# Kernel tuning notes

Hardware: AMD Instinct MI355X
Metric: run time of the kernel (lower is better)

## Reference

```python
import jax, jax.numpy as jnp
import numpy as np

B = 4096
IN_DIM = 256
OUT_DIM = 256
COND_DIM = 128
HID = 512
HYPER_OUT = IN_DIM * OUT_DIM  # 65536


def setup_inputs() -> dict:
    key = jax.random.key(0)
    ks = jax.random.split(key, 8)

    def xavier(k, shape):
        fan_in, fan_out = shape[0], shape[1]
        std = np.sqrt(2.0 / (fan_in + fan_out))
        return jax.random.normal(k, shape, dtype=jnp.float32) * std

    return {
        "input_h": jax.random.normal(ks[0], (B, IN_DIM), dtype=jnp.float32),
        "condition_z": jax.random.normal(ks[1], (B, COND_DIM), dtype=jnp.float32),
        # hypernet: Linear(COND_DIM, HID) -> ReLU -> Linear(HID, HYPER_OUT)
        "W1": xavier(ks[2], (COND_DIM, HID)),
        "b1": jnp.zeros((HID,), dtype=jnp.float32),
        "W2": xavier(ks[3], (HID, HYPER_OUT)),
        "b2": jnp.zeros((HYPER_OUT,), dtype=jnp.float32),
        # static bias (use_bias=True, generate_bias=False)
        "bias": jnp.zeros((1, OUT_DIM), dtype=jnp.float32),
    }


def reference(input_h, condition_z, W1, b1, W2, b2, bias):
    # HyperNet MLP generates per-sample weight matrix
    hyp = jax.nn.relu(condition_z @ W1 + b1)          # [B, HID]
    weight_S = hyp @ W2 + b2                          # [B, IN*OUT]  (1 GB intermediate)
    weight_S = weight_S.reshape(-1, IN_DIM, OUT_DIM)  # [B, IN, OUT]
    # batched matmul: [B,1,IN] x [B,IN,OUT] -> [B,OUT]
    out = jnp.einsum("bi,bio->bo", input_h, weight_S)
    return out + bias
```

## Files before the change

kernel.cpp:

```cpp
#include <hip/hip_runtime.h>
#include <hip/hip_bf16.h>
#include <stdint.h>


typedef __bf16 bf16x8 __attribute__((ext_vector_type(8)));
typedef float  f32x4  __attribute__((ext_vector_type(4)));

#define KTILES     2052
#define TILE_BYTES 32768
#define HYPT_OFF   (9u*1024u*1024u)

__global__ void k_init_out(const float* __restrict__ bias, float* __restrict__ out) {
    int idx = blockIdx.x * 256 + threadIdx.x;
    out[idx] = bias[idx & 255];
}

__global__ void k_hypT(const float* __restrict__ z, const float* __restrict__ W1,
                       const float* __restrict__ b1, float* __restrict__ hypT) {
    int blk = blockIdx.x;
    int t   = threadIdx.x;
    if (blk == 128) {
#pragma unroll
        for (int r = 0; r < 8; ++r) hypT[(size_t)512*4096 + r*512 + t] = 1.0f;
        return;
    }
    __shared__ float zs[32][128];
    int b0 = blk * 32;
#pragma unroll
    for (int u = 0; u < 8; ++u) {
        int idx = u * 512 + t;
        zs[idx >> 7][idx & 127] = z[b0 * 128 + idx];
    }
    __syncthreads();
    float acc[32];
    float bk = b1[t];
#pragma unroll
    for (int b = 0; b < 32; ++b) acc[b] = bk;
    for (int c = 0; c < 128; ++c) {
        float w = W1[c * 512 + t];
#pragma unroll
        for (int b = 0; b < 32; ++b) acc[b] = fmaf(zs[b][c], w, acc[b]);
    }
    float* dst = hypT + (size_t)t * 4096 + b0;
#pragma unroll
    for (int v = 0; v < 8; ++v) {
        f32x4 o;
#pragma unroll
        for (int q = 0; q < 4; ++q) {
            float a = acc[v * 4 + q];
            o[q] = a > 0.f ? a : 0.f;
        }
        *(f32x4*)(dst + v * 4) = o;
    }
}

__global__ void k_pack(const float* __restrict__ W2, const float* __restrict__ b2,
                       uint16_t* __restrict__ Bp) {
    __shared__ char tile[TILE_BYTES];
    int t   = blockIdx.x;
    int tid = threadIdx.x;
    long row0 = (long)t * 64;
    const float* src = (t < 2048) ? (W2 + row0 * 256) : (b2 + (row0 - 131072) * 256);
#pragma unroll
    for (int u = 0; u < 16; ++u) {
        int f = (u * 256 + tid) * 4;
        f32x4 v = *(const f32x4*)(src + f);
        int kk = f >> 8;
        int o0 = f & 255;
#pragma unroll
        for (int j = 0; j < 4; ++j) {
            int o = o0 + j;
            int addr = (o * 128 + kk * 2) ^ ((o & 7) << 4);
            *(__bf16*)(tile + addr) = (__bf16)v[j];
        }
    }
    __syncthreads();
    char* dst = (char*)Bp + (size_t)t * TILE_BYTES;
#pragma unroll
    for (int v = 0; v < 8; ++v) {
        int off = (v * 256 + tid) * 16;
        *(f32x4*)(dst + off) = *(const f32x4*)(tile + off);
    }
}

__global__ __launch_bounds__(512, 2) void k_gemm(
        const float* __restrict__ h, const float* __restrict__ hypT,
        const uint16_t* __restrict__ Bp, float* __restrict__ out) {
    __shared__ char smem[131072];

    const int tid  = threadIdx.x;
    const int lane = tid & 63;
    const int wid  = tid >> 6;
    const int wm   = wid >> 2, wn = wid & 3;
    const int l15  = lane & 15, lg = lane >> 4;

    const int bid = blockIdx.x;
    const int s   = bid & 7;
    const int mt  = bid >> 3;
    const int k0  = s * 64;
    const int row_base = mt * 128;
    const int NT  = (s == 7) ? 260 : 256;

    float* shyp = (float*)(smem + 98304);

#pragma unroll
    for (int u = 0; u < 4; ++u) {
        int f  = (u * 512 + tid) * 4;
        int kk = f >> 7;
        int r  = f & 127;
        *(f32x4*)(shyp + kk * 128 + r) =
            *(const f32x4*)(hypT + (size_t)(k0 + kk) * 4096 + row_base + r);
    }

    auto tile_of = [&](int idx) {
        return (idx < 256) ? ((k0 + (idx & 63)) * 4 + (idx >> 6)) : (2048 + idx - 256);
    };
    auto stage = [&](int bufoff, int t) {
        const char* gsrc = (const char*)Bp + (size_t)t * TILE_BYTES + wid * 4096 + lane * 16;
        char* ldst = smem + bufoff + wid * 4096;
#pragma unroll
        for (int q = 0; q < 4; ++q)
            __builtin_amdgcn_global_load_lds(
                (const __attribute__((address_space(1))) void*)(gsrc + q * 1024),
                (__attribute__((address_space(3))) void*)(ldst + q * 1024), 16, 0, 0);
    };

    stage(0,     tile_of(0));
    stage(32768, tile_of(1));
    asm volatile("s_waitcnt vmcnt(4) lgkmcnt(0)" ::: "memory");
    __builtin_amdgcn_s_barrier();

    f32x4 acc[4][4];
#pragma unroll
    for (int i = 0; i < 4; ++i)
#pragma unroll
        for (int j = 0; j < 4; ++j)
#pragma unroll
            for (int q = 0; q < 4; ++q) acc[i][j][q] = 0.0f;

    const f32x4 fzero = {0.f, 0.f, 0.f, 0.f};
    int boff_read = 0, boff_next = 32768, boff_stage = 65536;

    for (int G = 0; G < 8; ++G) {
        if (G >= 4 && s != 7) break;
        int niter = (G < 4) ? 64 : 1;

        bf16x8 af[4][2];
#pragma unroll
        for (int mf = 0; mf < 4; ++mf)
#pragma unroll
            for (int ks = 0; ks < 2; ++ks) {
                const float* hp = h + (size_t)(row_base + wm * 64 + mf * 16 + l15) * 256
                                    + (G & 3) * 64 + ks * 32 + lg * 8;
                f32x4 a = *(const f32x4*)hp, b = *(const f32x4*)(hp + 4);
                bf16x8 v;
                v[0] = (__bf16)a[0]; v[1] = (__bf16)a[1]; v[2] = (__bf16)a[2]; v[3] = (__bf16)a[3];
                v[4] = (__bf16)b[0]; v[5] = (__bf16)b[1]; v[6] = (__bf16)b[2]; v[7] = (__bf16)b[3];
                af[mf][ks] = v;
            }

        for (int jj = 0; jj < niter; ++jj) {
            int idx = (G < 4) ? G * 64 + jj : 256 + (G - 4);

            const char* sB = smem + boff_read;
            bf16x8 bf0[4], bf1[4];
#pragma unroll
            for (int nf = 0; nf < 4; ++nf) {
                int col = wn * 64 + nf * 16 + l15;
                int swz = (col & 7) << 4;
                bf0[nf] = *(const bf16x8*)(sB + ((col * 128 + lg * 16) ^ swz));
                bf1[nf] = *(const bf16x8*)(sB + ((col * 128 + 64 + lg * 16) ^ swz));
            }
            f32x4 scv[4];
            if (idx < 256) {
#pragma unroll
                for (int mf = 0; mf < 4; ++mf)
                    scv[mf] = *(const f32x4*)(shyp + jj * 128 + wm * 64 + mf * 16 + lg * 4);
            } else {
#pragma unroll
                for (int mf = 0; mf < 4; ++mf) scv[mf] = {1.f, 1.f, 1.f, 1.f};
            }

            bool do_stage = (idx + 2 < NT);
            if (do_stage) stage(boff_stage, tile_of(idx + 2));

            __builtin_amdgcn_s_setprio(1);
#pragma unroll
            for (int mf = 0; mf < 4; ++mf) {
                f32x4 part[4];
#pragma unroll
                for (int nf = 0; nf < 4; ++nf)
                    part[nf] = __builtin_amdgcn_mfma_f32_16x16x32_bf16(af[mf][0], bf0[nf], fzero, 0, 0, 0);
#pragma unroll
                for (int nf = 0; nf < 4; ++nf)
                    part[nf] = __builtin_amdgcn_mfma_f32_16x16x32_bf16(af[mf][1], bf1[nf], part[nf], 0, 0, 0);
#pragma unroll
                for (int nf = 0; nf < 4; ++nf)
#pragma unroll
                    for (int q = 0; q < 4; ++q)
                        acc[mf][nf][q] = fmaf(scv[mf][q], part[nf][q], acc[mf][nf][q]);
            }
            __builtin_amdgcn_s_setprio(0);

            if (do_stage) asm volatile("s_waitcnt vmcnt(4)" ::: "memory");
            else          asm volatile("s_waitcnt vmcnt(0)" ::: "memory");
            __builtin_amdgcn_s_barrier();

            int tmp = boff_read; boff_read = boff_next; boff_next = boff_stage; boff_stage = tmp;
        }
    }

    int crow0 = row_base + wm * 64;
    int ccol0 = wn * 64;
#pragma unroll
    for (int mf = 0; mf < 4; ++mf)
#pragma unroll
        for (int nf = 0; nf < 4; ++nf) {
            int col = ccol0 + nf * 16 + l15;
#pragma unroll
            for (int q = 0; q < 4; ++q) {
                int row = crow0 + mf * 16 + lg * 4 + q;
                atomicAdd(&out[row * 256 + col], acc[mf][nf][q]);
            }
        }
}

extern "C" void kernel_launch(void* const* d_in, const int* in_sizes, int n_in,
                              void* d_out, int out_size, void* d_ws, size_t ws_size,
                              hipStream_t stream) {
    const float* h    = (const float*)d_in[0];
    const float* z    = (const float*)d_in[1];
    const float* W1   = (const float*)d_in[2];
    const float* b1   = (const float*)d_in[3];
    const float* W2   = (const float*)d_in[4];
    const float* b2   = (const float*)d_in[5];
    const float* bias = (const float*)d_in[6];
    float* out = (float*)d_out;

    float*    hypT = (float*)d_ws;
    uint16_t* Bp   = (uint16_t*)((char*)d_ws + HYPT_OFF);

    k_pack    <<<KTILES, 256, 0, stream>>>(W2, b2, Bp);
    k_hypT    <<<129,    512, 0, stream>>>(z, W1, b1, hypT);
    k_init_out<<<4096,   256, 0, stream>>>(bias, out);
    k_gemm    <<<256,    512, 0, stream>>>(h, hypT, Bp, out);
}
```

Baseline: 358.6 us.

## Pre-cast h to bf16 and remap warps to 128x32 column strips

Adds a small kernel that converts h to bf16 once, so the GEMM loads bf16 A fragments directly instead of converting fp32 per block. The warp tiling moves from a 2x4 grid of 64x64 tiles to eight warps that each own all 128 rows and a 32-column strip. Each warp now reads half as many B fragments from LDS, but holds twice as many A fragments in registers. The staging prefetch is issued earlier and an extra barrier is added before the MFMA block. The new layout raises register pressure under launch_bounds(512,2) and costs one more kernel launch.

Result: slower. 376.2 us (+4.9%).

```diff
diff --git a/kernel.cpp b/kernel.cpp
--- a/kernel.cpp
+++ b/kernel.cpp
@@ -8,11 +8,22 @@
 
 #define KTILES     2052
 #define TILE_BYTES 32768
-#define HYPT_OFF   (9u*1024u*1024u)
+#define HB_OFF     (9u*1024u*1024u)
+#define BP_OFF     (12u*1024u*1024u)
 
 __global__ void k_init_out(const float* __restrict__ bias, float* __restrict__ out) {
     int idx = blockIdx.x * 256 + threadIdx.x;
     out[idx] = bias[idx & 255];
+}
+
+__global__ void k_hcast(const float* __restrict__ h, uint16_t* __restrict__ hb) {
+    int i = (blockIdx.x * 256 + threadIdx.x) * 8;
+    f32x4 a = *(const f32x4*)(h + i);
+    f32x4 b = *(const f32x4*)(h + i + 4);
+    bf16x8 v;
+    v[0] = (__bf16)a[0]; v[1] = (__bf16)a[1]; v[2] = (__bf16)a[2]; v[3] = (__bf16)a[3];
+    v[4] = (__bf16)b[0]; v[5] = (__bf16)b[1]; v[6] = (__bf16)b[2]; v[7] = (__bf16)b[3];
+    *(bf16x8*)(hb + i) = v;
 }
 
 __global__ void k_hypT(const float* __restrict__ z, const float* __restrict__ W1,
@@ -84,14 +95,13 @@
 }
 
 __global__ __launch_bounds__(512, 2) void k_gemm(
-        const float* __restrict__ h, const float* __restrict__ hypT,
+        const uint16_t* __restrict__ hb, const float* __restrict__ hypT,
         const uint16_t* __restrict__ Bp, float* __restrict__ out) {
     __shared__ char smem[131072];
 
     const int tid  = threadIdx.x;
     const int lane = tid & 63;
     const int wid  = tid >> 6;
-    const int wm   = wid >> 2, wn = wid & 3;
     const int l15  = lane & 15, lg = lane >> 4;
 
     const int bid = blockIdx.x;
@@ -100,6 +110,7 @@
     const int k0  = s * 64;
     const int row_base = mt * 128;
     const int NT  = (s == 7) ? 260 : 256;
+    const int colw = wid * 32;
 
     float* shyp = (float*)(smem + 98304);
 
@@ -130,11 +141,11 @@
     asm volatile("s_waitcnt vmcnt(4) lgkmcnt(0)" ::: "memory");
     __builtin_amdgcn_s_barrier();
 
-    f32x4 acc[4][4];
-#pragma unroll
-    for (int i = 0; i < 4; ++i)
-#pragma unroll
-        for (int j = 0; j < 4; ++j)
+    f32x4 acc[8][2];
+#pragma unroll
+    for (int i = 0; i < 8; ++i)
+#pragma unroll
+        for (int j = 0; j < 2; ++j)
 #pragma unroll
             for (int q = 0; q < 4; ++q) acc[i][j][q] = 0.0f;
 
@@ -143,63 +154,55 @@
 
     for (int G = 0; G < 8; ++G) {
         if (G >= 4 && s != 7) break;
-        int niter = (G < 4) ? 64 : 1;
-
-        bf16x8 af[4][2];
-#pragma unroll
-        for (int mf = 0; mf < 4; ++mf)
-#pragma unroll
-            for (int ks = 0; ks < 2; ++ks) {
-                const float* hp = h + (size_t)(row_base + wm * 64 + mf * 16 + l15) * 256
-                                    + (G & 3) * 64 + ks * 32 + lg * 8;
-                f32x4 a = *(const f32x4*)hp, b = *(const f32x4*)(hp + 4);
-                bf16x8 v;
-                v[0] = (__bf16)a[0]; v[1] = (__bf16)a[1]; v[2] = (__bf16)a[2]; v[3] = (__bf16)a[3];
-                v[4] = (__bf16)b[0]; v[5] = (__bf16)b[1]; v[6] = (__bf16)b[2]; v[7] = (__bf16)b[3];
-                af[mf][ks] = v;
+        const int niter = (G < 4) ? 64 : 1;
+
+        bf16x8 af[8][2];
+#pragma unroll
+        for (int mf = 0; mf < 8; ++mf)
+#pragma unroll
+            for (int ks = 0; ks < 2; ++ks)
+                af[mf][ks] = *(const bf16x8*)(hb + (size_t)(row_base + mf * 16 + l15) * 256
+                                              + (G & 3) * 64 + ks * 32 + lg * 8);
+
+        for (int jj = 0; jj < niter; ++jj) {
+            const int idx = (G < 4) ? G * 64 + jj : 256 + (G - 4);
+            const bool do_stage = (idx + 2 < NT);
+            if (do_stage) stage(boff_stage, tile_of(idx + 2));
+
+            const char* sB = smem + boff_read;
+            bf16x8 b0[2], b1[2];
+#pragma unroll
+            for (int nf = 0; nf < 2; ++nf) {
+                int col = colw + nf * 16 + l15;
+                int swz = (col & 7) << 4;
+                b0[nf] = *(const bf16x8*)(sB + ((col * 128 + lg * 16) ^ swz));
+                b1[nf] = *(const bf16x8*)(sB + ((col * 128 + 64 + lg * 16) ^ swz));
             }
-
-        for (int jj = 0; jj < niter; ++jj) {
-            int idx = (G < 4) ? G * 64 + jj : 256 + (G - 4);
-
-            const char* sB = smem + boff_read;
-            bf16x8 bf0[4], bf1[4];
-#pragma unroll
-            for (int nf = 0; nf < 4; ++nf) {
-                int col = wn * 64 + nf * 16 + l15;
-                int swz = (col & 7) << 4;
-                bf0[nf] = *(const bf16x8*)(sB + ((col * 128 + lg * 16) ^ swz));
-                bf1[nf] = *(const bf16x8*)(sB + ((col * 128 + 64 + lg * 16) ^ swz));
+            f32x4 scv[8];
+            if (idx < 256) {
+#pragma unroll
+                for (int mf = 0; mf < 8; ++mf)
+                    scv[mf] = *(const f32x4*)(shyp + jj * 128 + mf * 16 + lg * 4);
+            } else {
+#pragma unroll
+                for (int mf = 0; mf < 8; ++mf) scv[mf] = {1.f, 1.f, 1.f, 1.f};
             }
-            f32x4 scv[4];
-            if (idx < 256) {
-#pragma unroll
-                for (int mf = 0; mf < 4; ++mf)
-                    scv[mf] = *(const f32x4*)(shyp + jj * 128 + wm * 64 + mf * 16 + lg * 4);
-            } else {
-#pragma unroll
-                for (int mf = 0; mf < 4; ++mf) scv[mf] = {1.f, 1.f, 1.f, 1.f};
-            }
-
-            bool do_stage = (idx + 2 < NT);
-            if (do_stage) stage(boff_stage, tile_of(idx + 2));
+
+            asm volatile("" ::: "memory");
+            __builtin_amdgcn_s_barrier();
+            asm volatile("" ::: "memory");
 
             __builtin_amdgcn_s_setprio(1);
 #pragma unroll
-            for (int mf = 0; mf < 4; ++mf) {
-                f32x4 part[4];
-#pragma unroll
-                for (int nf = 0; nf < 4; ++nf)
-                    part[nf] = __builtin_amdgcn_mfma_f32_16x16x32_bf16(af[mf][0], bf0[nf], fzero, 0, 0, 0);
-#pragma unroll
-                for (int nf = 0; nf < 4; ++nf)
-                    part[nf] = __builtin_amdgcn_mfma_f32_16x16x32_bf16(af[mf][1], bf1[nf], part[nf], 0, 0, 0);
-#pragma unroll
-                for (int nf = 0; nf < 4; ++nf)
+            for (int mf = 0; mf < 8; ++mf)
+#pragma unroll
+                for (int nf = 0; nf < 2; ++nf) {
+                    f32x4 p = __builtin_amdgcn_mfma_f32_16x16x32_bf16(af[mf][0], b0[nf], fzero, 0, 0, 0);
+                    p = __builtin_amdgcn_mfma_f32_16x16x32_bf16(af[mf][1], b1[nf], p, 0, 0, 0);
 #pragma unroll
                     for (int q = 0; q < 4; ++q)
-                        acc[mf][nf][q] = fmaf(scv[mf][q], part[nf][q], acc[mf][nf][q]);
-            }
+                        acc[mf][nf][q] = fmaf(scv[mf][q], p[q], acc[mf][nf][q]);
+                }
             __builtin_amdgcn_s_setprio(0);
 
             if (do_stage) asm volatile("s_waitcnt vmcnt(4)" ::: "memory");
@@ -210,16 +213,14 @@
         }
     }
 
-    int crow0 = row_base + wm * 64;
-    int ccol0 = wn * 64;
-#pragma unroll
-    for (int mf = 0; mf < 4; ++mf)
-#pragma unroll
-        for (int nf = 0; nf < 4; ++nf) {
-            int col = ccol0 + nf * 16 + l15;
+#pragma unroll
+    for (int mf = 0; mf < 8; ++mf)
+#pragma unroll
+        for (int nf = 0; nf < 2; ++nf) {
+            int col = colw + nf * 16 + l15;
 #pragma unroll
             for (int q = 0; q < 4; ++q) {
-                int row = crow0 + mf * 16 + lg * 4 + q;
+                int row = row_base + mf * 16 + lg * 4 + q;
                 atomicAdd(&out[row * 256 + col], acc[mf][nf][q]);
             }
         }
@@ -238,10 +239,12 @@
     float* out = (float*)d_out;
 
     float*    hypT = (float*)d_ws;
-    uint16_t* Bp   = (uint16_t*)((char*)d_ws + HYPT_OFF);
+    uint16_t* hb   = (uint16_t*)((char*)d_ws + HB_OFF);
+    uint16_t* Bp   = (uint16_t*)((char*)d_ws + BP_OFF);
 
     k_pack    <<<KTILES, 256, 0, stream>>>(W2, b2, Bp);
     k_hypT    <<<129,    512, 0, stream>>>(z, W1, b1, hypT);
+    k_hcast   <<<512,    256, 0, stream>>>(h, hb);
     k_init_out<<<4096,   256, 0, stream>>>(bias, out);
-    k_gemm    <<<256,    512, 0, stream>>>(h, hypT, Bp, out);
-}
+    k_gemm    <<<256,    512, 0, stream>>>(hb, hypT, Bp, out);
+}
```

## Fold hypernet scale into f16 A operand and accumulate directly in MFMA

Applied to the files above, without the earlier changes.

Switches the packed weights and input from bf16 to fp16 and precasts h to fp16 in a separate kernel. The per-row hyper scale is now multiplied into the A fragments before the MFMAs, so the accumulator is fed straight through the MFMA chain. This removes the per-iteration fp32 FMA rescale of the partial products, and staging is issued earlier in the loop. In exchange it adds an extra cast kernel and fp16 range and precision risk on the scaled activations.

New measurement: 328.2 us. -8.5%, faster.

```diff
diff --git a/kernel.cpp b/kernel.cpp
--- a/kernel.cpp
+++ b/kernel.cpp
@@ -3,16 +3,27 @@
 #include <stdint.h>
 
 
-typedef __bf16 bf16x8 __attribute__((ext_vector_type(8)));
-typedef float  f32x4  __attribute__((ext_vector_type(4)));
+typedef _Float16 f16x8 __attribute__((ext_vector_type(8)));
+typedef float    f32x4 __attribute__((ext_vector_type(4)));
 
 #define KTILES     2052
 #define TILE_BYTES 32768
-#define HYPT_OFF   (9u*1024u*1024u)
+#define HB_OFF     (9u*1024u*1024u)
+#define BP_OFF     (12u*1024u*1024u)
 
 __global__ void k_init_out(const float* __restrict__ bias, float* __restrict__ out) {
     int idx = blockIdx.x * 256 + threadIdx.x;
     out[idx] = bias[idx & 255];
+}
+
+__global__ void k_hcast(const float* __restrict__ h, _Float16* __restrict__ hb) {
+    int i = (blockIdx.x * 256 + threadIdx.x) * 8;
+    f32x4 a = *(const f32x4*)(h + i);
+    f32x4 b = *(const f32x4*)(h + i + 4);
+    f16x8 v;
+    v[0] = (_Float16)a[0]; v[1] = (_Float16)a[1]; v[2] = (_Float16)a[2]; v[3] = (_Float16)a[3];
+    v[4] = (_Float16)b[0]; v[5] = (_Float16)b[1]; v[6] = (_Float16)b[2]; v[7] = (_Float16)b[3];
+    *(f16x8*)(hb + i) = v;
 }
 
 __global__ void k_hypT(const float* __restrict__ z, const float* __restrict__ W1,
@@ -55,7 +66,7 @@
 }
 
 __global__ void k_pack(const float* __restrict__ W2, const float* __restrict__ b2,
-                       uint16_t* __restrict__ Bp) {
+                       _Float16* __restrict__ Bp) {
     __shared__ char tile[TILE_BYTES];
     int t   = blockIdx.x;
     int tid = threadIdx.x;
@@ -71,7 +82,7 @@
         for (int j = 0; j < 4; ++j) {
             int o = o0 + j;
             int addr = (o * 128 + kk * 2) ^ ((o & 7) << 4);
-            *(__bf16*)(tile + addr) = (__bf16)v[j];
+            *(_Float16*)(tile + addr) = (_Float16)v[j];
         }
     }
     __syncthreads();
@@ -84,8 +95,8 @@
 }
 
 __global__ __launch_bounds__(512, 2) void k_gemm(
-        const float* __restrict__ h, const float* __restrict__ hypT,
-        const uint16_t* __restrict__ Bp, float* __restrict__ out) {
+        const _Float16* __restrict__ hb, const float* __restrict__ hypT,
+        const _Float16* __restrict__ Bp, float* __restrict__ out) {
     __shared__ char smem[131072];
 
     const int tid  = threadIdx.x;
@@ -138,67 +149,55 @@
 #pragma unroll
             for (int q = 0; q < 4; ++q) acc[i][j][q] = 0.0f;
 
-    const f32x4 fzero = {0.f, 0.f, 0.f, 0.f};
     int boff_read = 0, boff_next = 32768, boff_stage = 65536;
 
     for (int G = 0; G < 8; ++G) {
         if (G >= 4 && s != 7) break;
-        int niter = (G < 4) ? 64 : 1;
-
-        bf16x8 af[4][2];
+        const int niter = (G < 4) ? 64 : 1;
+
+        f16x8 af[4][2];
 #pragma unroll
         for (int mf = 0; mf < 4; ++mf)
 #pragma unroll
-            for (int ks = 0; ks < 2; ++ks) {
-                const float* hp = h + (size_t)(row_base + wm * 64 + mf * 16 + l15) * 256
-                                    + (G & 3) * 64 + ks * 32 + lg * 8;
-                f32x4 a = *(const f32x4*)hp, b = *(const f32x4*)(hp + 4);
-                bf16x8 v;
-                v[0] = (__bf16)a[0]; v[1] = (__bf16)a[1]; v[2] = (__bf16)a[2]; v[3] = (__bf16)a[3];
-                v[4] = (__bf16)b[0]; v[5] = (__bf16)b[1]; v[6] = (__bf16)b[2]; v[7] = (__bf16)b[3];
-                af[mf][ks] = v;
-            }
+            for (int ks = 0; ks < 2; ++ks)
+                af[mf][ks] = *(const f16x8*)(hb + (size_t)(row_base + wm * 64 + mf * 16 + l15) * 256
+                                             + (G & 3) * 64 + ks * 32 + lg * 8);
 
         for (int jj = 0; jj < niter; ++jj) {
-            int idx = (G < 4) ? G * 64 + jj : 256 + (G - 4);
+            const int idx = (G < 4) ? G * 64 + jj : 256 + (G - 4);
+            const bool do_stage = (idx + 2 < NT);
+            if (do_stage) stage(boff_stage, tile_of(idx + 2));
 
             const char* sB = smem + boff_read;
-            bf16x8 bf0[4], bf1[4];
+            f16x8 b0[4], b1[4];
 #pragma unroll
             for (int nf = 0; nf < 4; ++nf) {
                 int col = wn * 64 + nf * 16 + l15;
                 int swz = (col & 7) << 4;
-                bf0[nf] = *(const bf16x8*)(sB + ((col * 128 + lg * 16) ^ swz));
-                bf1[nf] = *(const bf16x8*)(sB + ((col * 128 + 64 + lg * 16) ^ swz));
-            }
-            f32x4 scv[4];
+                b0[nf] = *(const f16x8*)(sB + ((col * 128 + lg * 16) ^ swz));
+                b1[nf] = *(const f16x8*)(sB + ((col * 128 + 64 + lg * 16) ^ swz));
+            }
+            _Float16 sch[4];
             if (idx < 256) {
 #pragma unroll
                 for (int mf = 0; mf < 4; ++mf)
-                    scv[mf] = *(const f32x4*)(shyp + jj * 128 + wm * 64 + mf * 16 + lg * 4);
+                    sch[mf] = (_Float16)shyp[jj * 128 + wm * 64 + mf * 16 + l15];
             } else {
 #pragma unroll
-                for (int mf = 0; mf < 4; ++mf) scv[mf] = {1.f, 1.f, 1.f, 1.f};
-            }
-
-            bool do_stage = (idx + 2 < NT);
-            if (do_stage) stage(boff_stage, tile_of(idx + 2));
+                for (int mf = 0; mf < 4; ++mf) sch[mf] = (_Float16)1.0f;
+            }
 
             __builtin_amdgcn_s_setprio(1);
 #pragma unroll
             for (int mf = 0; mf < 4; ++mf) {
-                f32x4 part[4];
+                f16x8 as0 = af[mf][0] * sch[mf];
+                f16x8 as1 = af[mf][1] * sch[mf];
 #pragma unroll
                 for (int nf = 0; nf < 4; ++nf)
-                    part[nf] = __builtin_amdgcn_mfma_f32_16x16x32_bf16(af[mf][0], bf0[nf], fzero, 0, 0, 0);
+                    acc[mf][nf] = __builtin_amdgcn_mfma_f32_16x16x32_f16(as0, b0[nf], acc[mf][nf], 0, 0, 0);
 #pragma unroll
                 for (int nf = 0; nf < 4; ++nf)
-                    part[nf] = __builtin_amdgcn_mfma_f32_16x16x32_bf16(af[mf][1], bf1[nf], part[nf], 0, 0, 0);
-#pragma unroll
-                for (int nf = 0; nf < 4; ++nf)
-#pragma unroll
-                    for (int q = 0; q < 4; ++q)
-                        acc[mf][nf][q] = fmaf(scv[mf][q], part[nf][q], acc[mf][nf][q]);
+                    acc[mf][nf] = __builtin_amdgcn_mfma_f32_16x16x32_f16(as1, b1[nf], acc[mf][nf], 0, 0, 0);
             }
             __builtin_amdgcn_s_setprio(0);
 
@@ -237,11 +236,13 @@
     const float* bias = (const float*)d_in[6];
     float* out = (float*)d_out;
 
-    float*    hypT = (float*)d_ws;
-    uint16_t* Bp   = (uint16_t*)((char*)d_ws + HYPT_OFF);
+    float*     hypT = (float*)d_ws;
+    _Float16*  hb   = (_Float16*)((char*)d_ws + HB_OFF);
+    _Float16*  Bp   = (_Float16*)((char*)d_ws + BP_OFF);
 
     k_pack    <<<KTILES, 256, 0, stream>>>(W2, b2, Bp);
     k_hypT    <<<129,    512, 0, stream>>>(z, W1, b1, hypT);
+    k_hcast   <<<512,    256, 0, stream>>>(h, hb);
     k_init_out<<<4096,   256, 0, stream>>>(bias, out);
-    k_gemm    <<<256,    512, 0, stream>>>(h, hypT, Bp, out);
-}
+    k_gemm    <<<256,    512, 0, stream>>>(hb, hypT, Bp, out);
+}
```
